# Performance work log

Hardware: AMD Instinct MI355X
Metric: run time of the kernel (lower is better)

Reference implementation:

```python
import jax, jax.numpy as jnp
import numpy as np

N, E = 50000, 800000
IN_C, HID_C, OUT_C = 256, 256, 256


def setup_inputs() -> dict:
    key = jax.random.key(0)
    ks = jax.random.split(key, 8)
    x_piece = jax.random.normal(ks[0], (N, IN_C), dtype=jnp.float32)
    edge_index_piece = jax.random.randint(ks[1], (2, E), 0, N, dtype=jnp.int64)
    batch = jnp.zeros((N,), dtype=jnp.int64)
    def glorot(k, fan_in, fan_out):
        s = jnp.sqrt(6.0 / (fan_in + fan_out)).astype(jnp.float32)
        return jax.random.uniform(k, (fan_in, fan_out), jnp.float32, -s, s)
    return {
        "x_piece": x_piece,
        "edge_index_piece": edge_index_piece,
        "batch": batch,
        "W1": glorot(ks[2], IN_C, HID_C), "b1": jnp.zeros((HID_C,), jnp.float32),
        "W2": glorot(ks[3], HID_C, HID_C), "b2": jnp.zeros((HID_C,), jnp.float32),
        "W3": glorot(ks[4], HID_C, OUT_C), "b3": jnp.zeros((OUT_C,), jnp.float32),
    }


def _gcn_prep(edge_index, n_nodes):
    # add self-loops, compute symmetric normalization (PyG GCNConv default)
    src = jnp.concatenate([edge_index[0], jnp.arange(n_nodes, dtype=edge_index.dtype)])
    dst = jnp.concatenate([edge_index[1], jnp.arange(n_nodes, dtype=edge_index.dtype)])
    deg = jax.ops.segment_sum(jnp.ones_like(dst, dtype=jnp.float32), dst, num_segments=n_nodes)
    deg_inv_sqrt = jnp.where(deg > 0, jax.lax.rsqrt(jnp.maximum(deg, 1.0)), 0.0)
    norm = deg_inv_sqrt[src] * deg_inv_sqrt[dst]  # [E+N]
    return src, dst, norm


def _gcn_layer(x, src, dst, norm, W, b, n_nodes):
    h = x @ W                                   # [N, out] dense transform first
    msg = h[src] * norm[:, None]                # gather + scale
    out = jax.ops.segment_sum(msg, dst, num_segments=n_nodes)  # scatter-add
    return out + b


def reference(x_piece, edge_index_piece, batch, W1, b1, W2, b2, W3, b3):
    n_nodes = x_piece.shape[0]
    src, dst, norm = _gcn_prep(edge_index_piece, n_nodes)
    x = _gcn_layer(x_piece, src, dst, norm, W1, b1, n_nodes)
    x = jax.nn.gelu(x)
    x = _gcn_layer(x, src, dst, norm, W2, b2, n_nodes)
    x = jax.nn.gelu(x)
    x = _gcn_layer(x, src, dst, norm, W3, b3, n_nodes)
    return x
```

## Files before the change

### kernel.cpp

```cpp
#include <hip/hip_runtime.h>
#include <cstdint>
#include <cstddef>

#define CH 256

typedef _Float16 f16x8 __attribute__((ext_vector_type(8)));
typedef _Float16 f16x4 __attribute__((ext_vector_type(4)));
typedef float f32x4 __attribute__((ext_vector_type(4)));
typedef short short8 __attribute__((ext_vector_type(8)));

#define GLOB(x) ((const __attribute__((address_space(1))) void*)(x))
#define LDSP(x) ((__attribute__((address_space(3))) void*)(x))


__device__ __forceinline__ int ld_idx(const void* p, long long i, int w64) {
    if (w64) return (int)((const long long*)p)[i];
    return ((const int*)p)[i];
}

__device__ __forceinline__ float gelu_f(float x) {
    float x3 = x * x * x;
    float t = tanhf(0.7978845608028654f * (x + 0.044715f * x3));
    return 0.5f * x * (1.0f + t);
}

__device__ __forceinline__ int detect_w64(const void* ei, int E, int* sflag) {
    int tid = threadIdx.x;
    if (tid < 64) {
        long long k = ((long long)tid * (long long)(E - 1)) / 63;
        int w = ((const int*)ei)[2 * k + 1];
        unsigned long long vote = __ballot(w == 0);
        if (tid == 0) *sflag = (vote == ~0ULL) ? 1 : 0;
    }
    __syncthreads();
    return *sflag;
}


__global__ __launch_bounds__(256)
void k_pre(const float* __restrict__ x,
           const float* __restrict__ W1, const float* __restrict__ W2,
           const float* __restrict__ W3,
           int* __restrict__ deg, int* __restrict__ cnt,
           uint8_t* __restrict__ Xa, float* __restrict__ sxa,
           _Float16* __restrict__ Wh1, _Float16* __restrict__ Wh2,
           _Float16* __restrict__ Wh3, int N) {
    const int tid   = threadIdx.x;
    const int gsize = gridDim.x * 256;
    const int gid0  = blockIdx.x * 256 + tid;

    for (int i = gid0; i < N; i += gsize) { deg[i] = 0; cnt[i] = 0; }

    for (int i = gid0; i < 3 * CH * CH; i += gsize) {
        int l = i >> 16;
        int r = i & 65535;
        const float* W = (l == 0) ? W1 : (l == 1) ? W2 : W3;
        _Float16*   Wh = (l == 0) ? Wh1 : (l == 1) ? Wh2 : Wh3;
        Wh[r] = (_Float16)W[(r & 255) * CH + (r >> 8)];
    }

    int wave = gid0 >> 6, lane = tid & 63;
    int nwaves = gsize >> 6;
    for (int node = wave; node < N; node += nwaves) {
        float4 v = ((const float4*)(x + (size_t)node * CH))[lane];
        float mx = fmaxf(fmaxf(fabsf(v.x), fabsf(v.y)), fmaxf(fabsf(v.z), fabsf(v.w)));
        #pragma unroll
        for (int off = 32; off > 0; off >>= 1)
            mx = fmaxf(mx, __shfl_xor(mx, off));
        float inv = (mx > 0.f) ? (32767.0f / mx) : 0.f;
        short4 q;
        q.x = (short)__float2int_rn(v.x * inv);
        q.y = (short)__float2int_rn(v.y * inv);
        q.z = (short)__float2int_rn(v.z * inv);
        q.w = (short)__float2int_rn(v.w * inv);
        *(short4*)(Xa + (size_t)node * 512 + (size_t)lane * 8) = q;
        if (lane == 0) sxa[node] = mx * (1.0f / 32767.0f);
    }
}


__global__ void k_deg(const void* __restrict__ ei, int* __restrict__ deg, int E) {
    __shared__ int sflag;
    int w64 = detect_w64(ei, E, &sflag);
    int e = blockIdx.x * blockDim.x + threadIdx.x;
    if (e >= E) return;
    int d = ld_idx(ei, (long long)E + e, w64);
    atomicAdd(&deg[d], 1);
}

__global__ void k_scan_block(const int* __restrict__ deg, int* __restrict__ rowptr,
                             int* __restrict__ partial, int N) {
    __shared__ int s[256];
    int gid = blockIdx.x * 256 + threadIdx.x;
    int v = (gid < N) ? deg[gid] : 0;
    s[threadIdx.x] = v;
    __syncthreads();
    for (int off = 1; off < 256; off <<= 1) {
        int t = (threadIdx.x >= off) ? s[threadIdx.x - off] : 0;
        __syncthreads();
        s[threadIdx.x] += t;
        __syncthreads();
    }
    if (gid < N) rowptr[gid] = s[threadIdx.x] - v;
    if (threadIdx.x == 255) partial[blockIdx.x] = s[255];
}

__global__ void k_scan_partial(int* __restrict__ partial, int nb) {
    __shared__ int s[256];
    int i = threadIdx.x;
    int v = (i < nb) ? partial[i] : 0;
    s[i] = v;
    __syncthreads();
    for (int off = 1; off < 256; off <<= 1) {
        int t = (i >= off) ? s[i - off] : 0;
        __syncthreads();
        s[i] += t;
        __syncthreads();
    }
    if (i < nb) partial[i] = s[i] - v;
}

__global__ void k_add_off(int* __restrict__ rowptr, const int* __restrict__ partial,
                          const int* __restrict__ deg, float* __restrict__ dis,
                          int N, int E) {
    int gid = blockIdx.x * 256 + threadIdx.x;
    if (gid < N) {
        rowptr[gid] += partial[blockIdx.x];
        dis[gid] = 1.0f / sqrtf((float)(deg[gid] + 1));
    }
    if (gid == 0) rowptr[N] = E;
}

__global__ void k_scatter(const void* __restrict__ ei, const int* __restrict__ rowptr,
                          int* __restrict__ cnt, int* __restrict__ ssrc, int E) {
    __shared__ int sflag;
    int w64 = detect_w64(ei, E, &sflag);
    int e = blockIdx.x * blockDim.x + threadIdx.x;
    if (e >= E) return;
    int s = ld_idx(ei, e, w64);
    int d = ld_idx(ei, (long long)E + e, w64);
    int pos = rowptr[d] + atomicAdd(&cnt[d], 1);
    ssrc[pos] = s;
}


#define GM 128
#define GN 128
#define GK 32

__global__ __launch_bounds__(256, 2)
void k_gemm16(const uint8_t* __restrict__ X16, const float* __restrict__ sx,
              const _Float16* __restrict__ Bh, const float* __restrict__ dis,
              uint8_t* __restrict__ H16, float* __restrict__ hcomb, int M) {
    __shared__ __align__(16) char smem[65536];
    short*    lA16 = (short*)smem;
    _Float16* lB   = (_Float16*)(smem + 16384);

    const int tid  = threadIdx.x;
    const int lane = tid & 63;
    const int wid  = tid >> 6;
    const int m0   = blockIdx.x * GM;
    const int n0   = blockIdx.y * GN;
    const int wm   = wid >> 1, wn = wid & 1;
    const int r15  = lane & 15, kg = lane >> 4;

    auto stage = [&](int buf, int k0) {
        #pragma unroll
        for (int c = 0; c < 4; c++) {
            int call = wid * 4 + c;
            int cc = call & 7;
            int L = cc * 64 + lane;
            int row = L >> 2, ch = L & 3;
            int sch = ch ^ ((row >> 1) & 3);
            if (call < 8) {
                int gr = m0 + row; gr = (gr < M) ? gr : (M - 1);
                const uint8_t* g = X16 + (size_t)gr * 512 + (size_t)k0 * 2 + (sch << 4);
                __builtin_amdgcn_global_load_lds(GLOB(g), LDSP(&lA16[buf * 4096 + L * 8]), 16, 0, 0);
            } else {
                const _Float16* g = Bh + (size_t)(n0 + row) * CH + k0 + (sch << 3);
                __builtin_amdgcn_global_load_lds(GLOB(g), LDSP(&lB[buf * 4096 + L * 8]), 16, 0, 0);
            }
        }
    };

    f32x4 acc[4][4];
    #pragma unroll
    for (int i = 0; i < 4; i++)
        #pragma unroll
        for (int n = 0; n < 4; n++)
            acc[i][n] = (f32x4){0.f, 0.f, 0.f, 0.f};

    stage(0, 0);
    __syncthreads();

    for (int ks = 0; ks < 8; ks++) {
        int cur = ks & 1;
        if (ks < 7) stage(cur ^ 1, (ks + 1) * GK);

        f16x8 aq[4], bh[4];
        #pragma unroll
        for (int i = 0; i < 4; i++) {
            int R = wm * 64 + i * 16 + r15;
            int p = kg ^ ((R >> 1) & 3);
            short8 q = *(const short8*)&lA16[cur * 4096 + R * 32 + p * 8];
            #pragma unroll
            for (int j = 0; j < 8; j++)
                aq[i][j] = (_Float16)q[j];
        }
        #pragma unroll
        for (int n = 0; n < 4; n++) {
            int C = wn * 64 + n * 16 + r15;
            int p = kg ^ ((C >> 1) & 3);
            bh[n] = *(const f16x8*)&lB[cur * 4096 + C * GK + p * 8];
        }
        #pragma unroll
        for (int i = 0; i < 4; i++)
            #pragma unroll
            for (int n = 0; n < 4; n++)
                acc[i][n] = __builtin_amdgcn_mfma_f32_16x16x32_f16(aq[i], bh[n], acc[i][n], 0, 0, 0);
        __syncthreads();
    }

    float sC[4][4];
    #pragma unroll
    for (int i = 0; i < 4; i++)
        #pragma unroll
        for (int r = 0; r < 4; r++) {
            int gr = m0 + wm * 64 + i * 16 + kg * 4 + r;
            sC[i][r] = sx[(gr < M) ? gr : (M - 1)];
        }
    #pragma unroll
    for (int i = 0; i < 4; i++)
        #pragma unroll
        for (int n = 0; n < 4; n++)
            #pragma unroll
            for (int r = 0; r < 4; r++)
                acc[i][n][r] *= sC[i][r];

    float mx = 0.f;
    #pragma unroll
    for (int i = 0; i < 4; i++)
        #pragma unroll
        for (int n = 0; n < 4; n++)
            #pragma unroll
            for (int r = 0; r < 4; r++)
                mx = fmaxf(mx, fabsf(acc[i][n][r]));
    #pragma unroll
    for (int off = 32; off > 0; off >>= 1)
        mx = fmaxf(mx, __shfl_xor(mx, off));
    if (lane == 0) ((float*)smem)[wid] = mx;
    __syncthreads();
    float tmax = fmaxf(fmaxf(((float*)smem)[0], ((float*)smem)[1]),
                       fmaxf(((float*)smem)[2], ((float*)smem)[3]));
    float scl = tmax * (1.0f / 32767.0f);
    float inv = (tmax > 0.f) ? (32767.0f / tmax) : 0.f;
    __syncthreads();

    float* ep = (float*)smem + wid * 4096;
    #pragma unroll
    for (int i = 0; i < 4; i++)
        #pragma unroll
        for (int n = 0; n < 4; n++)
            #pragma unroll
            for (int r = 0; r < 4; r++)
                ep[(i * 16 + kg * 4 + r) * 64 + n * 16 + r15] = acc[i][n][r];
    __syncthreads();

    int q = lane & 15;
    int rsub = lane >> 4;
    #pragma unroll
    for (int p = 0; p < 16; p++) {
        int lrow = p * 4 + rsub;
        int grow = m0 + wm * 64 + lrow;
        if (grow < M) {
            int q0 = __float2int_rn(ep[lrow * 64 + q * 4 + 0] * inv);
            int q1 = __float2int_rn(ep[lrow * 64 + q * 4 + 1] * inv);
            int q2 = __float2int_rn(ep[lrow * 64 + q * 4 + 2] * inv);
            int q3 = __float2int_rn(ep[lrow * 64 + q * 4 + 3] * inv);
            uint2 d;
            d.x = (q0 & 0xFFFF) | (q1 << 16);
            d.y = (q2 & 0xFFFF) | (q3 << 16);
            int col = n0 + wn * 64 + q * 4;
            *(uint2*)(H16 + (size_t)grow * 512 + (size_t)col * 2) = d;
        }
    }

    if (tid < GM && m0 + tid < M)
        hcomb[(size_t)(m0 + tid) * 2 + (n0 >> 7)] = scl * dis[m0 + tid];
}


template <int MODE>
__global__ __launch_bounds__(256) void k_agg(const uint8_t* __restrict__ H16,
                                             const float* __restrict__ hcomb,
                                             const float* __restrict__ dis,
                                             const int* __restrict__ rowptr,
                                             const int* __restrict__ ssrc,
                                             const float* __restrict__ bias,
                                             float* __restrict__ out,
                                             uint8_t* __restrict__ Xout,
                                             float* __restrict__ sxout, int N) {
    int node = blockIdx.x * 4 + threadIdx.y;
    if (node >= N) return;
    int lane = threadIdx.x;
    int half = lane >> 5;
    float d = dis[node];
    short4 hv = *(const short4*)(H16 + (size_t)node * 512 + (size_t)lane * 8);
    float wself = d * hcomb[(size_t)node * 2 + half];
    float ax = wself * (float)hv.x, ay = wself * (float)hv.y;
    float az = wself * (float)hv.z, aw = wself * (float)hv.w;
    int s = rowptr[node], e = rowptr[node + 1];
    int j = s;
    for (; j + 8 <= e; j += 8) {
        int p[8];
        #pragma unroll
        for (int t = 0; t < 8; t++) p[t] = ssrc[j + t];
        short4 v[8];
        float sc[8];
        #pragma unroll
        for (int t = 0; t < 8; t++) {
            v[t] = *(const short4*)(H16 + (size_t)p[t] * 512 + (size_t)lane * 8);
            sc[t] = hcomb[(size_t)p[t] * 2 + half];
        }
        #pragma unroll
        for (int t = 0; t < 8; t++) {
            float wn = d * sc[t];
            ax += wn * (float)v[t].x; ay += wn * (float)v[t].y;
            az += wn * (float)v[t].z; aw += wn * (float)v[t].w;
        }
    }
    for (; j < e; j++) {
        int p = ssrc[j];
        float wn = d * hcomb[(size_t)p * 2 + half];
        short4 v = *(const short4*)(H16 + (size_t)p * 512 + (size_t)lane * 8);
        ax += wn * (float)v.x; ay += wn * (float)v.y;
        az += wn * (float)v.z; aw += wn * (float)v.w;
    }
    float4 b = ((const float4*)bias)[lane];
    ax += b.x; ay += b.y; az += b.z; aw += b.w;
    if (MODE == 0) {
        ax = gelu_f(ax); ay = gelu_f(ay); az = gelu_f(az); aw = gelu_f(aw);
        float mx = fmaxf(fmaxf(fabsf(ax), fabsf(ay)), fmaxf(fabsf(az), fabsf(aw)));
        #pragma unroll
        for (int off = 32; off > 0; off >>= 1)
            mx = fmaxf(mx, __shfl_xor(mx, off));
        float inv = (mx > 0.f) ? (32767.0f / mx) : 0.f;
        short4 q;
        q.x = (short)__float2int_rn(ax * inv);
        q.y = (short)__float2int_rn(ay * inv);
        q.z = (short)__float2int_rn(az * inv);
        q.w = (short)__float2int_rn(aw * inv);
        *(short4*)(Xout + (size_t)node * 512 + (size_t)lane * 8) = q;
        if (lane == 0) sxout[node] = mx * (1.0f / 32767.0f);
    } else {
        ((float4*)(out + (size_t)node * CH))[lane] = make_float4(ax, ay, az, aw);
    }
}


extern "C" void kernel_launch(void* const* d_in, const int* in_sizes, int n_in,
                              void* d_out, int out_size, void* d_ws, size_t ws_size,
                              hipStream_t stream) {
    const float* x  = (const float*)d_in[0];
    const void*  ei = d_in[1];
    const float* W1 = (const float*)d_in[3]; const float* b1 = (const float*)d_in[4];
    const float* W2 = (const float*)d_in[5]; const float* b2 = (const float*)d_in[6];
    const float* W3 = (const float*)d_in[7]; const float* b3 = (const float*)d_in[8];

    int N = in_sizes[0] / CH;
    int E = in_sizes[1] / 2;
    float* out = (float*)d_out;

    char* ws = (char*)d_ws;
    auto take = [&](size_t bytes) {
        char* p = ws;
        ws += (bytes + 15) & ~(size_t)15;
        return p;
    };
    uint8_t*  H16    = (uint8_t*) take((size_t)N * 512);
    uint8_t*  Xa     = (uint8_t*) take((size_t)N * 512);
    uint8_t*  Xb     = (uint8_t*) take((size_t)N * 512);
    float*    hcomb  = (float*)   take((size_t)N * 2 * sizeof(float));
    float*    sxa    = (float*)   take((size_t)N * sizeof(float));
    float*    sxb    = (float*)   take((size_t)N * sizeof(float));
    int*      deg    = (int*)     take((size_t)N * sizeof(int));
    float*    dis    = (float*)   take((size_t)N * sizeof(float));
    int*      rowptr = (int*)     take((size_t)(N + 1) * sizeof(int));
    int*      cnt    = (int*)     take((size_t)N * sizeof(int));
    int*      part   = (int*)     take(4096);
    int*      ssrc   = (int*)     take((size_t)E * sizeof(int));
    _Float16* Wh1    = (_Float16*)take((size_t)CH * CH * 2);
    _Float16* Wh2    = (_Float16*)take((size_t)CH * CH * 2);
    _Float16* Wh3    = (_Float16*)take((size_t)CH * CH * 2);

    int eb = (E + 255) / 256;
    int nb = (N + 255) / 256;

    k_pre<<<2048, 256, 0, stream>>>(x, W1, W2, W3, deg, cnt, Xa, sxa, Wh1, Wh2, Wh3, N);

    k_deg<<<eb, 256, 0, stream>>>(ei, deg, E);
    k_scan_block<<<nb, 256, 0, stream>>>(deg, rowptr, part, N);
    k_scan_partial<<<1, 256, 0, stream>>>(part, nb);
    k_add_off<<<nb, 256, 0, stream>>>(rowptr, part, deg, dis, N, E);
    k_scatter<<<eb, 256, 0, stream>>>(ei, rowptr, cnt, ssrc, E);

    dim3 ggrid((N + GM - 1) / GM, CH / GN);
    dim3 agrid((N + 3) / 4);
    dim3 ablock(64, 4);

    k_gemm16<<<ggrid, 256, 0, stream>>>(Xa, sxa, Wh1, dis, H16, hcomb, N);
    k_agg<0><<<agrid, ablock, 0, stream>>>(H16, hcomb, dis, rowptr, ssrc, b1, out, Xb, sxb, N);
    k_gemm16<<<ggrid, 256, 0, stream>>>(Xb, sxb, Wh2, dis, H16, hcomb, N);
    k_agg<0><<<agrid, ablock, 0, stream>>>(H16, hcomb, dis, rowptr, ssrc, b2, out, Xa, sxa, N);
    k_gemm16<<<ggrid, 256, 0, stream>>>(Xa, sxa, Wh3, dis, H16, hcomb, N);
    k_agg<1><<<agrid, ablock, 0, stream>>>(H16, hcomb, dis, rowptr, ssrc, b3, out, Xb, sxb, N);
}
```

Before: 373.1 us.

## Process two nodes per wavefront in aggregation with 16-byte row loads

The aggregation kernel now maps each 64-lane wavefront to two nodes, 32 lanes per node, and each lane loads 16 bytes (8 int16 values) per neighbor instead of 8 bytes. The grid is halved to match, the max reduction becomes a 32-wide shuffle, and the neighbor unroll drops from 8 to 4. The aim is wider memory transactions and more independent rows in flight per wavefront for the gather-bound scatter-add. In exchange, each lane holds more accumulator registers, and two nodes with different degrees now share a wavefront, which can cause divergence.

```diff
diff --git a/kernel.cpp b/kernel.cpp
--- a/kernel.cpp
+++ b/kernel.cpp
@@ -300,60 +300,72 @@
                                              float* __restrict__ out,
                                              uint8_t* __restrict__ Xout,
                                              float* __restrict__ sxout, int N) {
-    int node = blockIdx.x * 4 + threadIdx.y;
+    int lane = threadIdx.x;
+    int sub  = lane >> 5;
+    int node = blockIdx.x * 8 + threadIdx.y * 2 + sub;
     if (node >= N) return;
-    int lane = threadIdx.x;
-    int half = lane >> 5;
+    int cl   = lane & 31;
+    int half = cl >> 4;
     float d = dis[node];
-    short4 hv = *(const short4*)(H16 + (size_t)node * 512 + (size_t)lane * 8);
+
+    short8 hv = *(const short8*)(H16 + (size_t)node * 512 + (size_t)cl * 16);
     float wself = d * hcomb[(size_t)node * 2 + half];
-    float ax = wself * (float)hv.x, ay = wself * (float)hv.y;
-    float az = wself * (float)hv.z, aw = wself * (float)hv.w;
+    float a[8];
+    #pragma unroll
+    for (int k = 0; k < 8; k++) a[k] = wself * (float)hv[k];
+
     int s = rowptr[node], e = rowptr[node + 1];
     int j = s;
-    for (; j + 8 <= e; j += 8) {
-        int p[8];
-        #pragma unroll
-        for (int t = 0; t < 8; t++) p[t] = ssrc[j + t];
-        short4 v[8];
-        float sc[8];
-        #pragma unroll
-        for (int t = 0; t < 8; t++) {
-            v[t] = *(const short4*)(H16 + (size_t)p[t] * 512 + (size_t)lane * 8);
+    for (; j + 4 <= e; j += 4) {
+        int p[4];
+        #pragma unroll
+        for (int t = 0; t < 4; t++) p[t] = ssrc[j + t];
+        short8 v[4];
+        float sc[4];
+        #pragma unroll
+        for (int t = 0; t < 4; t++) {
+            v[t] = *(const short8*)(H16 + (size_t)p[t] * 512 + (size_t)cl * 16);
             sc[t] = hcomb[(size_t)p[t] * 2 + half];
         }
         #pragma unroll
-        for (int t = 0; t < 8; t++) {
+        for (int t = 0; t < 4; t++) {
             float wn = d * sc[t];
-            ax += wn * (float)v[t].x; ay += wn * (float)v[t].y;
-            az += wn * (float)v[t].z; aw += wn * (float)v[t].w;
+            #pragma unroll
+            for (int k = 0; k < 8; k++) a[k] += wn * (float)v[t][k];
         }
     }
     for (; j < e; j++) {
         int p = ssrc[j];
         float wn = d * hcomb[(size_t)p * 2 + half];
-        short4 v = *(const short4*)(H16 + (size_t)p * 512 + (size_t)lane * 8);
-        ax += wn * (float)v.x; ay += wn * (float)v.y;
-        az += wn * (float)v.z; aw += wn * (float)v.w;
-    }
-    float4 b = ((const float4*)bias)[lane];
-    ax += b.x; ay += b.y; az += b.z; aw += b.w;
+        short8 v = *(const short8*)(H16 + (size_t)p * 512 + (size_t)cl * 16);
+        #pragma unroll
+        for (int k = 0; k < 8; k++) a[k] += wn * (float)v[k];
+    }
+
+    float4 b0 = ((const float4*)bias)[cl * 2];
+    float4 b1 = ((const float4*)bias)[cl * 2 + 1];
+    a[0] += b0.x; a[1] += b0.y; a[2] += b0.z; a[3] += b0.w;
+    a[4] += b1.x; a[5] += b1.y; a[6] += b1.z; a[7] += b1.w;
+
     if (MODE == 0) {
-        ax = gelu_f(ax); ay = gelu_f(ay); az = gelu_f(az); aw = gelu_f(aw);
-        float mx = fmaxf(fmaxf(fabsf(ax), fabsf(ay)), fmaxf(fabsf(az), fabsf(aw)));
-        #pragma unroll
-        for (int off = 32; off > 0; off >>= 1)
-            mx = fmaxf(mx, __shfl_xor(mx, off));
+        #pragma unroll
+        for (int k = 0; k < 8; k++) a[k] = gelu_f(a[k]);
+        float mx = 0.f;
+        #pragma unroll
+        for (int k = 0; k < 8; k++) mx = fmaxf(mx, fabsf(a[k]));
+        #pragma unroll
+        for (int off = 16; off > 0; off >>= 1)
+            mx = fmaxf(mx, __shfl_xor(mx, off, 32));
         float inv = (mx > 0.f) ? (32767.0f / mx) : 0.f;
-        short4 q;
-        q.x = (short)__float2int_rn(ax * inv);
-        q.y = (short)__float2int_rn(ay * inv);
-        q.z = (short)__float2int_rn(az * inv);
-        q.w = (short)__float2int_rn(aw * inv);
-        *(short4*)(Xout + (size_t)node * 512 + (size_t)lane * 8) = q;
-        if (lane == 0) sxout[node] = mx * (1.0f / 32767.0f);
+        short8 q;
+        #pragma unroll
+        for (int k = 0; k < 8; k++) q[k] = (short)__float2int_rn(a[k] * inv);
+        *(short8*)(Xout + (size_t)node * 512 + (size_t)cl * 16) = q;
+        if (cl == 0) sxout[node] = mx * (1.0f / 32767.0f);
     } else {
-        ((float4*)(out + (size_t)node * CH))[lane] = make_float4(ax, ay, az, aw);
+        float* o = out + (size_t)node * CH + cl * 8;
+        *(f32x4*)o       = (f32x4){a[0], a[1], a[2], a[3]};
+        *(f32x4*)(o + 4) = (f32x4){a[4], a[5], a[6], a[7]};
     }
 }
 
@@ -405,7 +417,7 @@
     k_scatter<<<eb, 256, 0, stream>>>(ei, rowptr, cnt, ssrc, E);
 
     dim3 ggrid((N + GM - 1) / GM, CH / GN);
-    dim3 agrid((N + 3) / 4);
+    dim3 agrid((N + 7) / 8);
     dim3 ablock(64, 4);
 
     k_gemm16<<<ggrid, 256, 0, stream>>>(Xa, sxa, Wh1, dis, H16, hcomb, N);
```

After: 365.9 us. About the same (-1.9%).
